# Performance work log

Hardware: AMD Instinct MI355X
Metric: run time of the kernel (lower is better)

Reference implementation:

```python
import jax, jax.numpy as jnp
import numpy as np

DIM = 2048
N_HEAD = 32
N_KV = 8
HEAD_DIM = DIM // N_HEAD  # 64
GROUP = N_HEAD // N_KV    # 4


def setup_inputs() -> dict:
    key = jax.random.key(0)
    k1, k2, k3, k4 = jax.random.split(key, 4)
    B, S = 2, 2048
    x = jax.random.normal(k1, (B, S, DIM), dtype=jnp.float32)
    freqs_cis = jax.random.normal(k2, (S, HEAD_DIM // 2, 2), dtype=jnp.float32)
    wqkv_w = jax.random.normal(k3, (DIM, (N_HEAD + 2 * N_KV) * HEAD_DIM), dtype=jnp.float32) * 0.02
    wo_w = jax.random.normal(k4, (DIM, DIM), dtype=jnp.float32) * 0.02
    return {"x": x, "freqs_cis": freqs_cis, "wqkv_w": wqkv_w, "wo_w": wo_w}


def apply_rotary_emb(x, freqs_cis):
    # x: (B, S, H, head_dim), freqs_cis: (S, head_dim//2, 2)
    B, S, H, D = x.shape
    xs = x.astype(jnp.float32).reshape(B, S, H, D // 2, 2)
    fc = freqs_cis.reshape(1, S, 1, D // 2, 2)
    real = xs[..., 0] * fc[..., 0] - xs[..., 1] * fc[..., 1]
    imag = xs[..., 1] * fc[..., 0] + xs[..., 0] * fc[..., 1]
    out = jnp.stack([real, imag], axis=-1).reshape(B, S, H, D)
    return out.astype(x.dtype)


def reference(x, freqs_cis, wqkv_w, wo_w):
    B, S, _ = x.shape
    kv_size = N_KV * HEAD_DIM
    qkv = x @ wqkv_w  # (B, S, (n_head+2*n_kv)*head_dim)
    xq = qkv[..., :DIM].reshape(B, S, N_HEAD, HEAD_DIM)
    xk = qkv[..., DIM:DIM + kv_size].reshape(B, S, N_KV, HEAD_DIM)
    xv = qkv[..., DIM + kv_size:].reshape(B, S, N_KV, HEAD_DIM)

    xq = apply_rotary_emb(xq, freqs_cis)
    xk = apply_rotary_emb(xk, freqs_cis)

    # GQA without materializing repeated KV heads:
    # q: (B, n_kv, group, S, d); k, v: (B, n_kv, S, d)
    q = xq.transpose(0, 2, 1, 3).reshape(B, N_KV, GROUP, S, HEAD_DIM)
    k = xk.transpose(0, 2, 1, 3)
    v = xv.transpose(0, 2, 1, 3)

    scale = 1.0 / jnp.sqrt(jnp.asarray(HEAD_DIM, dtype=q.dtype))
    scores = jnp.einsum('bkgqd,bkKd->bkgqK', q, k) * scale  # (B, n_kv, group, S, S)
    causal = jnp.tril(jnp.ones((S, S), dtype=bool))
    neg = jnp.asarray(jnp.finfo(scores.dtype).min, dtype=scores.dtype)
    scores = jnp.where(causal, scores, neg)
    probs = jax.nn.softmax(scores, axis=-1)
    out = jnp.einsum('bkgqK,bkKd->bkgqd', probs, v)  # (B, n_kv, group, S, d)
    out = out.reshape(B, N_HEAD, S, HEAD_DIM).transpose(0, 2, 1, 3).reshape(B, S, DIM)
    return out @ wo_w
```

## Files before the change

### kernel.cpp

```cpp
#include <hip/hip_runtime.h>
#include <hip/hip_bf16.h>
#include <math.h>

#define DIM 2048
#define NH 32
#define NKV 8
#define HD 64
#define SEQ 2048
#define BATCH 2
#define MTOT (BATCH*SEQ)
#define QKV_N ((NH + 2*NKV)*HD)
#define QSCALE 0.18033688011112042f

typedef __bf16 bf16x8 __attribute__((ext_vector_type(8)));
typedef float f32x4 __attribute__((ext_vector_type(4)));

#if __has_builtin(__builtin_amdgcn_exp2f)
#define EXP2F __builtin_amdgcn_exp2f
#else
#define EXP2F exp2f
#endif

__device__ __forceinline__ void gld_lds16(const void* g, void* l) {
  __builtin_amdgcn_global_load_lds((__attribute__((address_space(1))) void*)g,
                                   (__attribute__((address_space(3))) void*)l,
                                   16, 0, 0);
}

#define PHASE_SYNC4 asm volatile("s_waitcnt vmcnt(4)\n\ts_barrier" ::: "memory")
#define PHASE_SYNC0 asm volatile("s_waitcnt vmcnt(0)\n\ts_barrier" ::: "memory")
#define POST_SYNC   asm volatile("s_waitcnt lgkmcnt(0)\n\ts_barrier" ::: "memory")

__global__ void cvt_x_kernel(const float* __restrict__ src, __hip_bfloat16* __restrict__ dst, int n4) {
  int i = blockIdx.x * 256 + threadIdx.x;
  if (i >= n4) return;
  float4 v = ((const float4*)src)[i];
  union { __hip_bfloat16 h[4]; uint2 u; } t;
  t.h[0] = __float2bfloat16(v.x); t.h[1] = __float2bfloat16(v.y);
  t.h[2] = __float2bfloat16(v.z); t.h[3] = __float2bfloat16(v.w);
  ((uint2*)dst)[i] = t.u;
}

__global__ void transpose_cvt_kernel(const float* __restrict__ src, __hip_bfloat16* __restrict__ dst,
                                     int R, int C) {
  __shared__ float tile[32][33];
  int c0 = blockIdx.x * 32, r0 = blockIdx.y * 32;
  int tx = threadIdx.x & 31, ty = threadIdx.x >> 5;
  #pragma unroll
  for (int i = ty; i < 32; i += 8)
    tile[i][tx] = src[(size_t)(r0 + i) * C + c0 + tx];
  __syncthreads();
  #pragma unroll
  for (int i = ty; i < 32; i += 8)
    dst[(size_t)(c0 + i) * R + r0 + tx] = __float2bfloat16(tile[tx][i]);
}

__global__ __launch_bounds__(256) void gemm_qkv_rope_kernel(const __hip_bfloat16* __restrict__ A,
                                                            const __hip_bfloat16* __restrict__ Bt,
                                                            const float* __restrict__ freqs,
                                                            __hip_bfloat16* __restrict__ Qb,
                                                            __hip_bfloat16* __restrict__ Kb,
                                                            __hip_bfloat16* __restrict__ Vb) {
  __shared__ __hip_bfloat16 As[2][128 * 32];
  __shared__ __hip_bfloat16 Bs[2][128 * 32];
  const int tid = threadIdx.x;
  const int w = tid >> 6, lane = tid & 63, ln = lane & 15, quad = lane >> 4;
  const int wr = w >> 1, wc = w & 1;
  const int id = blockIdx.x;
  const int wg = (id & 7) * 96 + (id >> 3);
  const int bx = wg % 24, by = wg / 24;
  const int m0 = by * 128, n0 = bx * 128;
  const int K = DIM;
  const __hip_bfloat16* Ag = A + (size_t)(m0 + w * 16 + (lane >> 2)) * K + (lane & 3) * 8;
  const __hip_bfloat16* Bg = Bt + (size_t)(n0 + w * 16 + (lane >> 2)) * K + (lane & 3) * 8;
  f32x4 acc[4][4] = {};

  auto stage = [&](int buf, int k) {
    gld_lds16(Ag + k, &As[buf][w * 512]);
    gld_lds16(Ag + (size_t)64 * K + k, &As[buf][w * 512 + 2048]);
    gld_lds16(Bg + k, &Bs[buf][w * 512]);
    gld_lds16(Bg + (size_t)64 * K + k, &Bs[buf][w * 512 + 2048]);
  };
  auto compute = [&](int buf) {
    bf16x8 af[4], bf[4];
    #pragma unroll
    for (int i = 0; i < 4; i++)
      af[i] = *(const bf16x8*)&As[buf][(wr * 64 + i * 16 + ln) * 32 + quad * 8];
    #pragma unroll
    for (int j = 0; j < 4; j++)
      bf[j] = *(const bf16x8*)&Bs[buf][(wc * 64 + j * 16 + ln) * 32 + quad * 8];
    #pragma unroll
    for (int i = 0; i < 4; i++)
      #pragma unroll
      for (int j = 0; j < 4; j++)
        acc[i][j] = __builtin_amdgcn_mfma_f32_16x16x32_bf16(af[i], bf[j], acc[i][j], 0, 0, 0);
  };

  stage(0, 0);
  stage(1, 32);
  for (int k0 = 0; k0 + 64 < K; k0 += 64) {
    PHASE_SYNC4;
    compute(0);
    POST_SYNC;
    stage(0, k0 + 64);
    PHASE_SYNC4;
    compute(1);
    POST_SYNC;
    stage(1, k0 + 96);
  }
  PHASE_SYNC4;
  compute(0);
  PHASE_SYNC0;
  compute(1);

  const int region = (n0 >= 2560) ? 2 : (n0 >= 2048 ? 1 : 0);
  #pragma unroll
  for (int i = 0; i < 4; i++) {
    #pragma unroll
    for (int j = 0; j < 4; j++) {
      const int n = n0 + wc * 64 + j * 16 + ln;
      const int d = n & 63;
      #pragma unroll
      for (int r = 0; r < 4; r++) {
        const int m = m0 + wr * 64 + i * 16 + quad * 4 + r;
        const int bb = m >> 11, s = m & 2047;
        float v = acc[i][j][r];
        if (region == 2) {
          Vb[((size_t)(bb * NKV + ((n - 2560) >> 6)) * SEQ + s) * HD + d] = __float2bfloat16(v);
        } else {
          float p = __shfl_xor(v, 1);
          const float2 fc = *(const float2*)&freqs[s * 64 + (d & ~1)];
          float o = (d & 1) ? (v * fc.x + p * fc.y) : (v * fc.x - p * fc.y);
          if (region == 0)
            Qb[((size_t)(bb * NH + (n >> 6)) * SEQ + s) * HD + d] = __float2bfloat16(o * QSCALE);
          else
            Kb[((size_t)(bb * NKV + ((n - 2048) >> 6)) * SEQ + s) * HD + d] = __float2bfloat16(o);
        }
      }
    }
  }
}

__global__ __launch_bounds__(256) void gemm_wo_kernel(const __hip_bfloat16* __restrict__ A,
                                                      const __hip_bfloat16* __restrict__ Bt,
                                                      float* __restrict__ C) {
  __shared__ __hip_bfloat16 As[2][128 * 32];
  __shared__ __hip_bfloat16 Bs[2][128 * 32];
  const int tid = threadIdx.x;
  const int w = tid >> 6, lane = tid & 63, ln = lane & 15, quad = lane >> 4;
  const int wr = w >> 1, wc = w & 1;
  const int id = blockIdx.x;
  const int wg = (id & 7) * 64 + (id >> 3);
  const int bx = wg & 15, by = wg >> 4;
  const int m0 = by * 128, n0 = bx * 128;
  const int K = DIM, N = DIM;
  const __hip_bfloat16* Ag = A + (size_t)(m0 + w * 16 + (lane >> 2)) * K + (lane & 3) * 8;
  const __hip_bfloat16* Bg = Bt + (size_t)(n0 + w * 16 + (lane >> 2)) * K + (lane & 3) * 8;
  f32x4 acc[4][4] = {};

  auto stage = [&](int buf, int k) {
    gld_lds16(Ag + k, &As[buf][w * 512]);
    gld_lds16(Ag + (size_t)64 * K + k, &As[buf][w * 512 + 2048]);
    gld_lds16(Bg + k, &Bs[buf][w * 512]);
    gld_lds16(Bg + (size_t)64 * K + k, &Bs[buf][w * 512 + 2048]);
  };
  auto compute = [&](int buf) {
    bf16x8 af[4], bf[4];
    #pragma unroll
    for (int i = 0; i < 4; i++)
      af[i] = *(const bf16x8*)&As[buf][(wr * 64 + i * 16 + ln) * 32 + quad * 8];
    #pragma unroll
    for (int j = 0; j < 4; j++)
      bf[j] = *(const bf16x8*)&Bs[buf][(wc * 64 + j * 16 + ln) * 32 + quad * 8];
    #pragma unroll
    for (int i = 0; i < 4; i++)
      #pragma unroll
      for (int j = 0; j < 4; j++)
        acc[i][j] = __builtin_amdgcn_mfma_f32_16x16x32_bf16(af[i], bf[j], acc[i][j], 0, 0, 0);
  };

  stage(0, 0);
  stage(1, 32);
  for (int k0 = 0; k0 + 64 < K; k0 += 64) {
    PHASE_SYNC4;
    compute(0);
    POST_SYNC;
    stage(0, k0 + 64);
    PHASE_SYNC4;
    compute(1);
    POST_SYNC;
    stage(1, k0 + 96);
  }
  PHASE_SYNC4;
  compute(0);
  PHASE_SYNC0;
  compute(1);

  #pragma unroll
  for (int i = 0; i < 4; i++) {
    const int r0 = m0 + wr * 64 + i * 16 + quad * 4;
    #pragma unroll
    for (int j = 0; j < 4; j++) {
      const int cc = n0 + wc * 64 + j * 16 + ln;
      #pragma unroll
      for (int r = 0; r < 4; r++)
        C[(size_t)(r0 + r) * N + cc] = acc[i][j][r];
    }
  }
}

__global__ __launch_bounds__(256, 3) void attn_kernel(const __hip_bfloat16* __restrict__ Q,
                                                      const __hip_bfloat16* __restrict__ Kg,
                                                      const __hip_bfloat16* __restrict__ Vg,
                                                      __hip_bfloat16* __restrict__ O) {
  __shared__ __hip_bfloat16 Ks[128 * 64];
  __shared__ __hip_bfloat16 Vs[64 * 136];
  __shared__ __hip_bfloat16 Ps[4][32 * 72];
  const int id = blockIdx.x;
  const int xcd = id & 7, slot = id >> 3;
  const int cmb = xcd * 2 + (slot >> 6);
  const int b = cmb >> 3, kvh = cmb & 7;
  const int s_ = slot & 63;
  const int t = 15 - (s_ >> 2);
  const int h = kvh * 4 + (s_ & 3);
  const int tid = threadIdx.x, w = tid >> 6, lane = tid & 63, ln = lane & 15, quad = lane >> 4;
  const size_t qbase = (size_t)(b * NH + h) * SEQ * HD;
  const size_t kbase = (size_t)(b * NKV + kvh) * SEQ * HD;

  const __hip_bfloat16* Kgl = Kg + kbase + (size_t)(tid >> 3) * 64 + (size_t)(((tid & 7) ^ ((tid >> 3) & 7)) * 8);
  const int vrow = tid >> 2, vcb = (tid & 3) * 16, vsw = (tid & 3) << 4;
  const int psw = ((ln >> 2) & 3) << 4;

  const int qgw = t * 128 + w * 32;
  bf16x8 qf[2][2];
  #pragma unroll
  for (int f = 0; f < 2; f++)
    #pragma unroll
    for (int kt = 0; kt < 2; kt++)
      qf[f][kt] = *(const bf16x8*)(Q + qbase + (size_t)(qgw + f * 16 + ln) * HD + kt * 32 + quad * 8);
  f32x4 Oacc[2][4] = {};
  float lrow[2][4] = {};
  union { unsigned short u[8]; bf16x8 v; } onesu;
  #pragma unroll
  for (int i = 0; i < 8; i++) onesu.u[i] = 0x3F80;
  const bf16x8 ones = onesu.v;

  uint4 vd[2][2];
  #pragma unroll
  for (int bt = 0; bt < 2; bt++)
    #pragma unroll
    for (int cc = 0; cc < 2; cc++)
      vd[bt][cc] = *(const uint4*)(Vg + kbase + (size_t)(bt * 64 + vrow) * HD + vcb + cc * 8);

  for (int j = 0; j <= t; j++) {
    #pragma unroll
    for (int c = 0; c < 4; c++)
      gld_lds16(Kgl + (size_t)j * 8192 + c * 2048, &Ks[c * 2048 + w * 512]);
    #pragma unroll
    for (int bt = 0; bt < 2; bt++)
      #pragma unroll
      for (int cc = 0; cc < 2; cc++) {
        const __hip_bfloat16* vp = (const __hip_bfloat16*)&vd[bt][cc];
        const int col = vcb + cc * 8;
        const int sr = (bt * 64 + vrow) ^ vsw;
        #pragma unroll
        for (int e = 0; e < 8; e++)
          Vs[(col + e) * 136 + sr] = vp[e];
      }
    __syncthreads();
    if (j < t) {
      #pragma unroll
      for (int bt = 0; bt < 2; bt++)
        #pragma unroll
        for (int cc = 0; cc < 2; cc++)
          vd[bt][cc] = *(const uint4*)(Vg + kbase + (size_t)((j + 1) * 128 + bt * 64 + vrow) * HD + vcb + cc * 8);
    }
    const bool lastIter = (j == t);
    #pragma unroll
    for (int s2 = 0; s2 < 2; s2++) {
      if (lastIter && s2 * 64 > w * 32 + 31) continue;
      bf16x8 kf[4][2];
      #pragma unroll
      for (int nt = 0; nt < 4; nt++)
        #pragma unroll
        for (int kt = 0; kt < 2; kt++) {
          const int kv = s2 * 64 + nt * 16 + ln;
          kf[nt][kt] = *(const bf16x8*)&Ks[(kv * 8 + ((kt * 4 + quad) ^ (ln & 7))) * 8];
        }
      #pragma unroll
      for (int f = 0; f < 2; f++) {
        if (lastIter && s2 * 64 > w * 32 + f * 16 + 15) continue;
        f32x4 sf[4];
        #pragma unroll
        for (int nt = 0; nt < 4; nt++) {
          f32x4 s = {};
          s = __builtin_amdgcn_mfma_f32_16x16x32_bf16(qf[f][0], kf[nt][0], s, 0, 0, 0);
          s = __builtin_amdgcn_mfma_f32_16x16x32_bf16(qf[f][1], kf[nt][1], s, 0, 0, 0);
          sf[nt] = s;
        }
        if (lastIter && s2 * 64 + 63 > w * 32 + f * 16) {
          const int qr = w * 32 + f * 16 + quad * 4;
          #pragma unroll
          for (int nt = 0; nt < 4; nt++) {
            const int kg = s2 * 64 + nt * 16 + ln;
            #pragma unroll
            for (int r = 0; r < 4; r++)
              if (kg > qr + r) sf[nt][r] = -1.0e38f;
          }
        }
        #pragma unroll
        for (int nt = 0; nt < 4; nt++)
          #pragma unroll
          for (int r = 0; r < 4; r++)
            Ps[w][(f * 16 + quad * 4 + r) * 72 + ((nt * 16 + ln) ^ (quad << 4))] =
                __float2bfloat16(EXP2F(sf[nt][r]));
      }
      #pragma unroll
      for (int f = 0; f < 2; f++) {
        if (lastIter && s2 * 64 > w * 32 + f * 16 + 15) continue;
        f32x4 ls = {};
        #pragma unroll
        for (int kt = 0; kt < 2; kt++) {
          bf16x8 pf = *(const bf16x8*)&Ps[w][(f * 16 + ln) * 72 + ((kt * 32 + quad * 8) ^ psw)];
          ls = __builtin_amdgcn_mfma_f32_16x16x32_bf16(pf, ones, ls, 0, 0, 0);
          #pragma unroll
          for (int dt = 0; dt < 4; dt++) {
            bf16x8 vf = *(const bf16x8*)&Vs[(dt * 16 + ln) * 136 + s2 * 64 + ((kt * 32 + quad * 8) ^ (dt << 4))];
            Oacc[f][dt] = __builtin_amdgcn_mfma_f32_16x16x32_bf16(pf, vf, Oacc[f][dt], 0, 0, 0);
          }
        }
        #pragma unroll
        for (int r = 0; r < 4; r++) lrow[f][r] += ls[r];
      }
    }
    __syncthreads();
  }
  #pragma unroll
  for (int f = 0; f < 2; f++) {
    const int so = qgw + f * 16 + quad * 4;
    #pragma unroll
    for (int r = 0; r < 4; r++) {
      const float inv = 1.0f / lrow[f][r];
      #pragma unroll
      for (int dt = 0; dt < 4; dt++)
        O[((size_t)(b * SEQ) + so + r) * DIM + h * HD + dt * 16 + ln] =
            __float2bfloat16(Oacc[f][dt][r] * inv);
    }
  }
}

extern "C" void kernel_launch(void* const* d_in, const int* in_sizes, int n_in,
                              void* d_out, int out_size, void* d_ws, size_t ws_size,
                              hipStream_t stream) {
  const float* x     = (const float*)d_in[0];
  const float* freqs = (const float*)d_in[1];
  const float* wqkv  = (const float*)d_in[2];
  const float* wo    = (const float*)d_in[3];
  float* out = (float*)d_out;

  char* ws = (char*)d_ws;
  __hip_bfloat16* xb    = (__hip_bfloat16*)ws; ws += (size_t)MTOT * DIM * 2;
  __hip_bfloat16* wqkvT = (__hip_bfloat16*)ws; ws += (size_t)QKV_N * DIM * 2;
  __hip_bfloat16* woT   = (__hip_bfloat16*)ws; ws += (size_t)DIM * DIM * 2;
  __hip_bfloat16* Qb    = (__hip_bfloat16*)ws; ws += (size_t)BATCH * NH * SEQ * HD * 2;
  __hip_bfloat16* Kb    = (__hip_bfloat16*)ws; ws += (size_t)BATCH * NKV * SEQ * HD * 2;
  __hip_bfloat16* Vb    = (__hip_bfloat16*)ws; ws += (size_t)BATCH * NKV * SEQ * HD * 2;
  __hip_bfloat16* attnb = (__hip_bfloat16*)ws; ws += (size_t)MTOT * DIM * 2;

  cvt_x_kernel<<<(MTOT * DIM / 4 + 255) / 256, 256, 0, stream>>>(x, xb, MTOT * DIM / 4);
  transpose_cvt_kernel<<<dim3(QKV_N / 32, DIM / 32), 256, 0, stream>>>(wqkv, wqkvT, DIM, QKV_N);
  transpose_cvt_kernel<<<dim3(DIM / 32, DIM / 32), 256, 0, stream>>>(wo, woT, DIM, DIM);
  gemm_qkv_rope_kernel<<<768, 256, 0, stream>>>(xb, wqkvT, freqs, Qb, Kb, Vb);
  attn_kernel<<<1024, 256, 0, stream>>>(Qb, Kb, Vb, attnb);
  gemm_wo_kernel<<<512, 256, 0, stream>>>(attnb, woT, out);
}
```

Baseline: 313.2 us.

## Rewrite QKV GEMM with 256x256 tiles, 8 waves, swizzled LDS and interleaved pipeline

The QKV+RoPE GEMM now uses 256x256 output tiles with 512 threads (8 waves, 2x4 layout), a 64-wide K step, and an XOR-swizzled LDS layout to reduce bank conflicts. Global-to-LDS staging of the next K tile is interleaved with four MFMA sub-phases separated by barriers, and s_setprio is raised around the MFMA blocks. The aim is more data reuse per tile and better overlap of loads with compute. The trade-off is that only 192 blocks are launched on a 256-CU device, which can leave CUs idle, and register pressure from 32 accumulators per wave goes up.

```diff
diff --git a/kernel.cpp b/kernel.cpp
--- a/kernel.cpp
+++ b/kernel.cpp
@@ -27,6 +27,9 @@
                                    16, 0, 0);
 }
 
+#define MIDBAR     asm volatile("s_barrier" ::: "memory")
+#define ENDBAR     asm volatile("s_barrier" ::: "memory")
+#define ENDBAR_VM0 asm volatile("s_waitcnt vmcnt(0)\n\ts_barrier" ::: "memory")
 #define PHASE_SYNC4 asm volatile("s_waitcnt vmcnt(4)\n\ts_barrier" ::: "memory")
 #define PHASE_SYNC0 asm volatile("s_waitcnt vmcnt(0)\n\ts_barrier" ::: "memory")
 #define POST_SYNC   asm volatile("s_waitcnt lgkmcnt(0)\n\ts_barrier" ::: "memory")
@@ -55,76 +58,93 @@
     dst[(size_t)(c0 + i) * R + r0 + tx] = __float2bfloat16(tile[tx][i]);
 }
 
-__global__ __launch_bounds__(256) void gemm_qkv_rope_kernel(const __hip_bfloat16* __restrict__ A,
-                                                            const __hip_bfloat16* __restrict__ Bt,
-                                                            const float* __restrict__ freqs,
-                                                            __hip_bfloat16* __restrict__ Qb,
-                                                            __hip_bfloat16* __restrict__ Kb,
-                                                            __hip_bfloat16* __restrict__ Vb) {
-  __shared__ __hip_bfloat16 As[2][128 * 32];
-  __shared__ __hip_bfloat16 Bs[2][128 * 32];
+__global__ __launch_bounds__(512, 2) void gemm_qkv_rope_kernel(const __hip_bfloat16* __restrict__ A,
+                                                               const __hip_bfloat16* __restrict__ Bt,
+                                                               const float* __restrict__ freqs,
+                                                               __hip_bfloat16* __restrict__ Qb,
+                                                               __hip_bfloat16* __restrict__ Kb,
+                                                               __hip_bfloat16* __restrict__ Vb) {
+  __shared__ __hip_bfloat16 lds[65536];
   const int tid = threadIdx.x;
   const int w = tid >> 6, lane = tid & 63, ln = lane & 15, quad = lane >> 4;
-  const int wr = w >> 1, wc = w & 1;
+  const int wr = w >> 2, wc = w & 3;
   const int id = blockIdx.x;
-  const int wg = (id & 7) * 96 + (id >> 3);
-  const int bx = wg % 24, by = wg / 24;
-  const int m0 = by * 128, n0 = bx * 128;
+  const int wg = (id & 7) * 24 + (id >> 3);
+  const int bx = wg % 12, by = wg / 12;
+  const int m0 = by * 256, n0 = bx * 256;
   const int K = DIM;
-  const __hip_bfloat16* Ag = A + (size_t)(m0 + w * 16 + (lane >> 2)) * K + (lane & 3) * 8;
-  const __hip_bfloat16* Bg = Bt + (size_t)(n0 + w * 16 + (lane >> 2)) * K + (lane & 3) * 8;
-  f32x4 acc[4][4] = {};
-
-  auto stage = [&](int buf, int k) {
-    gld_lds16(Ag + k, &As[buf][w * 512]);
-    gld_lds16(Ag + (size_t)64 * K + k, &As[buf][w * 512 + 2048]);
-    gld_lds16(Bg + k, &Bs[buf][w * 512]);
-    gld_lds16(Bg + (size_t)64 * K + k, &Bs[buf][w * 512 + 2048]);
-  };
-  auto compute = [&](int buf) {
-    bf16x8 af[4], bf[4];
-    #pragma unroll
-    for (int i = 0; i < 4; i++)
-      af[i] = *(const bf16x8*)&As[buf][(wr * 64 + i * 16 + ln) * 32 + quad * 8];
-    #pragma unroll
-    for (int j = 0; j < 4; j++)
-      bf[j] = *(const bf16x8*)&Bs[buf][(wc * 64 + j * 16 + ln) * 32 + quad * 8];
-    #pragma unroll
-    for (int i = 0; i < 4; i++)
-      #pragma unroll
-      for (int j = 0; j < 4; j++)
-        acc[i][j] = __builtin_amdgcn_mfma_f32_16x16x32_bf16(af[i], bf[j], acc[i][j], 0, 0, 0);
-  };
-
-  stage(0, 0);
-  stage(1, 32);
-  for (int k0 = 0; k0 + 64 < K; k0 += 64) {
-    PHASE_SYNC4;
-    compute(0);
-    POST_SYNC;
-    stage(0, k0 + 64);
-    PHASE_SYNC4;
-    compute(1);
-    POST_SYNC;
-    stage(1, k0 + 96);
-  }
-  PHASE_SYNC4;
-  compute(0);
-  PHASE_SYNC0;
-  compute(1);
+
+  const int swl  = (tid * 16) ^ (((tid >> 5) & 1) << 5);
+  const int srow = swl >> 6;
+  const int scol = (swl & 63) >> 1;
+  const __hip_bfloat16* Asrc = A  + (size_t)(m0 + srow) * K + scol;
+  const __hip_bfloat16* Bsrc = Bt + (size_t)(n0 + srow) * K + scol;
+  __hip_bfloat16* ldsw = &lds[w * 512];
+
+  const int acol = (quad * 8) ^ (((ln >> 3) & 1) << 4);
+
+#define SPA(b,h,kk) ((((b)*2 + (h))*2 + (kk)) * 4096)
+#define SPB(b,h,kk) (32768 + SPA(b,h,kk))
+#define STAGE_A(b,h,k) do { \
+    gld_lds16(Asrc + (size_t)((h)*128) * K + (k),      ldsw + SPA(b,h,0)); \
+    gld_lds16(Asrc + (size_t)((h)*128) * K + (k) + 32, ldsw + SPA(b,h,1)); } while (0)
+#define STAGE_B(b,h,k) do { \
+    gld_lds16(Bsrc + (size_t)((h)*128) * K + (k),      ldsw + SPB(b,h,0)); \
+    gld_lds16(Bsrc + (size_t)((h)*128) * K + (k) + 32, ldsw + SPB(b,h,1)); } while (0)
+
+  bf16x8 af[4][2], bf[2][2];
+  f32x4 acc[8][4] = {};
+
+#define LDA(b, mh) do { _Pragma("unroll") \
+    for (int i = 0; i < 4; i++) { \
+      af[i][0] = *(const bf16x8*)&lds[SPA(b, wr, 0) + (((mh)*4 + i)*16 + ln)*32 + acol]; \
+      af[i][1] = *(const bf16x8*)&lds[SPA(b, wr, 1) + (((mh)*4 + i)*16 + ln)*32 + acol]; } } while (0)
+#define LDB(b, nh) do { _Pragma("unroll") \
+    for (int j = 0; j < 2; j++) { \
+      bf[j][0] = *(const bf16x8*)&lds[SPB(b, wc>>1, 0) + ((wc&1)*64 + ((nh)*2 + j)*16 + ln)*32 + acol]; \
+      bf[j][1] = *(const bf16x8*)&lds[SPB(b, wc>>1, 1) + ((wc&1)*64 + ((nh)*2 + j)*16 + ln)*32 + acol]; } } while (0)
+#define MMAC(mh, nh) do { __builtin_amdgcn_s_setprio(1); \
+    _Pragma("unroll") for (int i = 0; i < 4; i++) \
+      _Pragma("unroll") for (int j = 0; j < 2; j++) { \
+        acc[(mh)*4+i][(nh)*2+j] = __builtin_amdgcn_mfma_f32_16x16x32_bf16(af[i][0], bf[j][0], acc[(mh)*4+i][(nh)*2+j], 0,0,0); \
+        acc[(mh)*4+i][(nh)*2+j] = __builtin_amdgcn_mfma_f32_16x16x32_bf16(af[i][1], bf[j][1], acc[(mh)*4+i][(nh)*2+j], 0,0,0); } \
+    __builtin_amdgcn_s_setprio(0); } while (0)
+
+  STAGE_A(0, 0, 0); STAGE_A(0, 1, 0); STAGE_B(0, 0, 0); STAGE_B(0, 1, 0);
+  ENDBAR_VM0;
+
+  for (int T = 0; T < 31; T++) {
+    const int b = T & 1, nb = b ^ 1;
+    const int k1 = (T + 1) * 64;
+    LDA(b, 0); LDB(b, 0);
+    STAGE_A(nb, 0, k1);
+    MIDBAR; MMAC(0, 0); ENDBAR;
+    LDB(b, 1);
+    STAGE_A(nb, 1, k1);
+    MIDBAR; MMAC(0, 1); ENDBAR;
+    LDA(b, 1);
+    STAGE_B(nb, 0, k1); STAGE_B(nb, 1, k1);
+    MIDBAR; MMAC(1, 1); ENDBAR;
+    LDB(b, 0);
+    MIDBAR; MMAC(1, 0); ENDBAR_VM0;
+  }
+  LDA(1, 0); LDB(1, 0); MIDBAR; MMAC(0, 0); ENDBAR;
+  LDB(1, 1);            MIDBAR; MMAC(0, 1); ENDBAR;
+  LDA(1, 1);            MIDBAR; MMAC(1, 1); ENDBAR;
+  LDB(1, 0);            MIDBAR; MMAC(1, 0);
 
   const int region = (n0 >= 2560) ? 2 : (n0 >= 2048 ? 1 : 0);
   #pragma unroll
-  for (int i = 0; i < 4; i++) {
-    #pragma unroll
-    for (int j = 0; j < 4; j++) {
-      const int n = n0 + wc * 64 + j * 16 + ln;
+  for (int mf = 0; mf < 8; mf++) {
+    #pragma unroll
+    for (int nf = 0; nf < 4; nf++) {
+      const int n = n0 + wc * 64 + nf * 16 + ln;
       const int d = n & 63;
       #pragma unroll
       for (int r = 0; r < 4; r++) {
-        const int m = m0 + wr * 64 + i * 16 + quad * 4 + r;
+        const int m = m0 + wr * 128 + mf * 16 + quad * 4 + r;
         const int bb = m >> 11, s = m & 2047;
-        float v = acc[i][j][r];
+        float v = acc[mf][nf][r];
         if (region == 2) {
           Vb[((size_t)(bb * NKV + ((n - 2560) >> 6)) * SEQ + s) * HD + d] = __float2bfloat16(v);
         } else {
@@ -139,6 +159,13 @@
       }
     }
   }
+#undef SPA
+#undef SPB
+#undef STAGE_A
+#undef STAGE_B
+#undef LDA
+#undef LDB
+#undef MMAC
 }
 
 __global__ __launch_bounds__(256) void gemm_wo_kernel(const __hip_bfloat16* __restrict__ A,
@@ -370,7 +397,7 @@
   cvt_x_kernel<<<(MTOT * DIM / 4 + 255) / 256, 256, 0, stream>>>(x, xb, MTOT * DIM / 4);
   transpose_cvt_kernel<<<dim3(QKV_N / 32, DIM / 32), 256, 0, stream>>>(wqkv, wqkvT, DIM, QKV_N);
   transpose_cvt_kernel<<<dim3(DIM / 32, DIM / 32), 256, 0, stream>>>(wo, woT, DIM, DIM);
-  gemm_qkv_rope_kernel<<<768, 256, 0, stream>>>(xb, wqkvT, freqs, Qb, Kb, Vb);
+  gemm_qkv_rope_kernel<<<192, 512, 0, stream>>>(xb, wqkvT, freqs, Qb, Kb, Vb);
   attn_kernel<<<1024, 256, 0, stream>>>(Qb, Kb, Vb, attnb);
   gemm_wo_kernel<<<512, 256, 0, stream>>>(attnb, woT, out);
 }
```

Result: slower. 333.6 us (+6.5%).
